# Kernel tuning notes

Hardware: AMD Instinct MI355X
Metric: run time of the kernel (lower is better)

The kernel has to match this reference:

```python
import jax, jax.numpy as jnp
import numpy as np

B, T, D, H = 2, 2048, 1024, 16
DH = D // H


def setup_inputs() -> dict:
    key = jax.random.key(0)
    ks = jax.random.split(key, 5)
    scale = 1.0 / np.sqrt(D)
    return {
        "x": jax.random.normal(ks[0], (B, T, D), dtype=jnp.float32),
        "Wq": jax.random.normal(ks[1], (D, D), dtype=jnp.float32) * scale,
        "Wk": jax.random.normal(ks[2], (D, D), dtype=jnp.float32) * scale,
        "Wv": jax.random.normal(ks[3], (D, D), dtype=jnp.float32) * scale,
        "Wo": jax.random.normal(ks[4], (D, D), dtype=jnp.float32) * scale,
    }


def _split(y):
    # (B,T,D) -> (B,H,T,DH)
    b, t, _ = y.shape
    return y.reshape(b, t, H, DH).transpose(0, 2, 1, 3)


def reference(x, Wq, Wk, Wv, Wo):
    q = _split(x @ Wq)
    k = _split(x @ Wk)
    v = _split(x @ Wv)
    scores = jnp.einsum("bhqd,bhkd->bhqk", q, k) / jnp.sqrt(jnp.float32(DH))
    t = x.shape[1]
    # additive causal mask: -1e9 above the diagonal (matches band_part logic)
    causal = jnp.tril(jnp.ones((t, t), dtype=jnp.float32))
    scores = scores + (1.0 - causal) * -1e9
    attn = jax.nn.softmax(scores, axis=-1)
    out = jnp.einsum("bhqk,bhkd->bhqd", attn, v)  # (B,H,T,DH)
    out = out.transpose(0, 2, 1, 3).reshape(x.shape[0], t, D)
    return out @ Wo
```

## Files before the change

kernel.cpp:

```cpp
#include <hip/hip_runtime.h>

#define BB 2
#define TT 2048
#define DD 1024
#define HH 16
#define DHD 64
#define MM (BB*TT)

typedef __attribute__((ext_vector_type(8))) short short8;
typedef __attribute__((ext_vector_type(4))) float float4v;
typedef unsigned short u16;

__device__ inline float bf2f(u16 u) {
    union { unsigned int i; float f; } v;
    v.i = ((unsigned int)u) << 16;
    return v.f;
}
__device__ inline u16 f2bf(float f) {
    union { float f; unsigned int i; } v;
    v.f = f;
    unsigned int x = v.i;
    unsigned int r = (x + 0x7fffu + ((x >> 16) & 1u)) >> 16;
    return (u16)r;
}

__device__ inline void gl_lds16(const u16* g, u16* l) {
    __builtin_amdgcn_global_load_lds(
        (const __attribute__((address_space(1))) unsigned int*)g,
        (__attribute__((address_space(3))) unsigned int*)l, 16, 0, 0);
}

__global__ __launch_bounds__(256) void prep_k(const float* __restrict__ x,
                                              const float* __restrict__ Wq,
                                              const float* __restrict__ Wk,
                                              const float* __restrict__ Wv,
                                              const float* __restrict__ Wo,
                                              u16* __restrict__ xb,
                                              u16* __restrict__ WT) {
    int tid = threadIdx.x;
    if (blockIdx.z == 4) {
        int bid = blockIdx.y * 32 + blockIdx.x;
#pragma unroll
        for (int k = 0; k < 4; k++) {
            int i = bid * 1024 + k * 256 + tid;
            float4v v = ((const float4v*)x)[i];
            ushort4 o;
            o.x = f2bf(v[0]); o.y = f2bf(v[1]); o.z = f2bf(v[2]); o.w = f2bf(v[3]);
            ((ushort4*)xb)[i] = o;
        }
        return;
    }
    __shared__ u16 t[32][33];
    int wsel = blockIdx.z;
    const float* W = (wsel == 0) ? Wq : (wsel == 1) ? Wk : (wsel == 2) ? Wv : Wo;
    u16* o = WT + (size_t)wsel * DD * DD;
    int k0 = blockIdx.y * 32, n0 = blockIdx.x * 32;
    int tx = tid & 31, ty = tid >> 5;
#pragma unroll
    for (int i = 0; i < 4; i++) {
        int k = ty + i * 8;
        t[k][tx] = f2bf(W[(size_t)(k0 + k) * DD + n0 + tx]);
    }
    __syncthreads();
#pragma unroll
    for (int i = 0; i < 4; i++) {
        int n = ty + i * 8;
        o[(size_t)(n0 + n) * DD + k0 + tx] = t[tx][n];
    }
}

template <int MODE, int TM, int TN, int BK>
__global__ __launch_bounds__(256) void gemm_k(const u16* __restrict__ A,
                                              const u16* __restrict__ WT0,
                                              void* __restrict__ outp) {
    const int K = DD;
    const int MT = TM / 32, NT = TN / 32;
    const int NS = (TM + TN) * (BK / 8) / 256;
    const int CPR = BK / 8;

    int z = blockIdx.z;
    const u16* WT = WT0 + (size_t)z * DD * DD;
    int n0 = blockIdx.x * TN, m0 = blockIdx.y * TM;

    __shared__ u16 S[(TM + TN) * BK];

    int tid = threadIdx.x;
    int lane = tid & 63, w = tid >> 6;
    int wm = (w >> 1) * (TM / 2), wn = (w & 1) * (TN / 2);
    int quad = lane >> 4, l16 = lane & 15;

    const u16* gp[NS];
    u16* lp[NS];
#pragma unroll
    for (int j = 0; j < NS; j++) {
        int cid = tid + j * 256;
        int r = cid / CPR, c = cid % CPR;
        lp[j] = S + (size_t)cid * 8;
        gp[j] = (r < TM ? A + (size_t)(m0 + r) * K
                        : WT + (size_t)(n0 + r - TM) * K) + ((c ^ (r & 7)) * 8);
    }
    int swz = l16 & 7;

    float4v acc[MT][NT];
#pragma unroll
    for (int i = 0; i < MT; i++)
#pragma unroll
        for (int j = 0; j < NT; j++) acc[i][j] = (float4v)(0.0f);

    const int NK = K / BK;
#pragma unroll 1
    for (int ki = 0; ki < NK; ki++) {
        __syncthreads();
#pragma unroll
        for (int j = 0; j < NS; j++)
            gl_lds16(gp[j] + ki * BK, lp[j]);
        __syncthreads();

#pragma unroll
        for (int ks = 0; ks < BK / 32; ks++) {
            int cq = ((ks * 4 + quad) ^ swz) * 8;
            short8 a[MT], b[NT];
#pragma unroll
            for (int mt = 0; mt < MT; mt++)
                a[mt] = *(const short8*)&S[(wm + mt * 16 + l16) * BK + cq];
#pragma unroll
            for (int nt = 0; nt < NT; nt++)
                b[nt] = *(const short8*)&S[(TM + wn + nt * 16 + l16) * BK + cq];
#pragma unroll
            for (int mt = 0; mt < MT; mt++)
#pragma unroll
                for (int nt = 0; nt < NT; nt++)
                    acc[mt][nt] = __builtin_amdgcn_mfma_f32_16x16x32_bf16(
                        a[mt], b[nt], acc[mt][nt], 0, 0, 0);
        }
    }

#pragma unroll
    for (int mt = 0; mt < MT; mt++) {
#pragma unroll
        for (int nt = 0; nt < NT; nt++) {
#pragma unroll
            for (int r = 0; r < 4; r++) {
                int m = m0 + wm + mt * 16 + quad * 4 + r;
                int n = n0 + wn + nt * 16 + l16;
                float v = acc[mt][nt][r];
                if constexpr (MODE == 0) {
                    int bb = m >> 11, t = m & 2047;
                    int h = n >> 6, dh = n & 63;
                    size_t idx;
                    if (z == 2)
                        idx = (((size_t)2 * BB * HH + bb * HH + h) * DHD + dh) * TT + t;
                    else
                        idx = (((size_t)z * BB * HH + bb * HH + h) * TT + t) * DHD + dh;
                    ((u16*)outp)[idx] = f2bf(v);
                } else {
                    ((float*)outp)[(size_t)m * DD + n] = v;
                }
            }
        }
    }
}

__global__ __launch_bounds__(512, 4) void attn_k(const u16* __restrict__ QKV,
                                                 u16* __restrict__ AO) {
    const u16* Q  = QKV;
    const u16* Kp = QKV + (size_t)MM * DD;
    const u16* Vp = QKV + (size_t)2 * MM * DD;
    int bh = blockIdx.x;
    int by = blockIdx.y;
    int qt = (by < 8) ? (15 - by) : (by - 8);
    size_t hoff = (size_t)bh * TT * DHD;

    __shared__ u16 Ks[2][2][64 * 64];
    __shared__ u16 VTs[2][2][64 * 64];
    __shared__ u16 Ps[8][16 * 64];

    int tid = threadIdx.x;
    int lane = tid & 63, wv = tid >> 6;
    int quad = lane >> 4, l16 = lane & 15;
    int cxs = l16 & 7;

    int sr = tid >> 3, sc = tid & 7;
    int sl = sr * 64 + ((sc ^ (sr & 7)) * 8);
    const u16* gK = Kp + hoff + (size_t)sr * DHD + sc * 8;
    const u16* gV = Vp + hoff + (size_t)sr * TT + sc * 8;

    const float qscale = 0.125f * 1.4426950408889634f;
    int q0 = qt * 128;
    int ql = wv * 16 + l16;
    short8 aq0, aq1;
    {
        const u16* gq = Q + hoff + (size_t)(q0 + ql) * DHD;
        short8 v0 = *(const short8*)(gq + quad * 8);
        short8 v1 = *(const short8*)(gq + 32 + quad * 8);
#pragma unroll
        for (int e = 0; e < 8; e++) {
            aq0[e] = (short)f2bf(bf2f((u16)v0[e]) * qscale);
            aq1[e] = (short)f2bf(bf2f((u16)v1[e]) * qscale);
        }
    }

    short8 prK[2], prV[2];
    prK[0] = *(const short8*)gK;
    prK[1] = *(const short8*)(gK + (size_t)64 * DHD);
    prV[0] = *(const short8*)gV;
    prV[1] = *(const short8*)(gV + 64);

    const int NR = qt + 1;

    float4v o[4];
#pragma unroll
    for (int i = 0; i < 4; i++) o[i] = (float4v)(0.0f);
    float lr = 0.0f;

#pragma unroll 1
    for (int jt = 0; jt < NR; jt++) {
        int db = jt & 1;
#pragma unroll
        for (int tt = 0; tt < 2; tt++) {
            *(short8*)&Ks[db][tt][sl]  = prK[tt];
            *(short8*)&VTs[db][tt][sl] = prV[tt];
        }
        __syncthreads();

        if (jt + 1 < NR) {
            size_t nj = (size_t)(jt + 1) * 128;
            prK[0] = *(const short8*)(gK + nj * DHD);
            prK[1] = *(const short8*)(gK + (nj + 64) * DHD);
            prV[0] = *(const short8*)(gV + nj);
            prV[1] = *(const short8*)(gV + nj + 64);
        }

#pragma unroll
        for (int tt = 0; tt < 2; tt++) {
            int lim = ql - tt * 64;
            if (jt == qt && lim < 0) continue;

            float4v s[4];
#pragma unroll
            for (int ct = 0; ct < 4; ct++) {
                int kr = (ct * 16 + l16) * 64;
                short8 ak0 = *(const short8*)&Ks[db][tt][kr + ((quad ^ cxs) * 8)];
                short8 ak1 = *(const short8*)&Ks[db][tt][kr + (((4 + quad) ^ cxs) * 8)];
                float4v sv = (float4v)(0.0f);
                sv = __builtin_amdgcn_mfma_f32_16x16x32_bf16(ak0, aq0, sv, 0, 0, 0);
                sv = __builtin_amdgcn_mfma_f32_16x16x32_bf16(ak1, aq1, sv, 0, 0, 0);
                s[ct] = sv;
            }

            if (jt == qt) {
#pragma unroll
                for (int ct = 0; ct < 4; ct++)
#pragma unroll
                    for (int r = 0; r < 4; r++) {
                        int kvl = ct * 16 + quad * 4 + r;
                        if (kvl > lim) s[ct][r] = -30000.0f;
                    }
            }

#pragma unroll
            for (int ct = 0; ct < 4; ct++) {
                float p0 = __builtin_amdgcn_exp2f(s[ct][0]);
                float p1 = __builtin_amdgcn_exp2f(s[ct][1]);
                float p2 = __builtin_amdgcn_exp2f(s[ct][2]);
                float p3 = __builtin_amdgcn_exp2f(s[ct][3]);
                lr += (p0 + p1) + (p2 + p3);
                union { float f; unsigned u; } c0, c1, c2, c3;
                c0.f = p0; c1.f = p1; c2.f = p2; c3.f = p3;
                ushort4 pw;
                pw.x = (u16)(c0.u >> 16);
                pw.y = (u16)(c1.u >> 16);
                pw.z = (u16)(c2.u >> 16);
                pw.w = (u16)(c3.u >> 16);
                int chnk = (ct * 2 + (quad >> 1)) ^ cxs;
                *(ushort4*)&Ps[wv][l16 * 64 + chnk * 8 + (quad & 1) * 4] = pw;
            }

            short8 ap0 = *(const short8*)&Ps[wv][l16 * 64 + ((quad ^ cxs) * 8)];
            short8 ap1 = *(const short8*)&Ps[wv][l16 * 64 + (((4 + quad) ^ cxs) * 8)];
#pragma unroll
            for (int ct = 0; ct < 4; ct++) {
                int vr = (ct * 16 + l16) * 64;
                short8 bv0 = *(const short8*)&VTs[db][tt][vr + ((quad ^ cxs) * 8)];
                short8 bv1 = *(const short8*)&VTs[db][tt][vr + (((4 + quad) ^ cxs) * 8)];
                o[ct] = __builtin_amdgcn_mfma_f32_16x16x32_bf16(ap0, bv0, o[ct], 0, 0, 0);
                o[ct] = __builtin_amdgcn_mfma_f32_16x16x32_bf16(ap1, bv1, o[ct], 0, 0, 0);
            }
        }
    }

    float rs = lr;
    rs += __shfl_xor(rs, 16);
    rs += __shfl_xor(rs, 32);
    int gbase = lane & 48;
    float rinv[4];
#pragma unroll
    for (int r = 0; r < 4; r++)
        rinv[r] = 1.0f / __shfl(rs, gbase + quad * 4 + r);

    int b = bh >> 4, h = bh & 15;
#pragma unroll
    for (int ct = 0; ct < 4; ct++) {
#pragma unroll
        for (int r = 0; r < 4; r++) {
            int q = q0 + wv * 16 + quad * 4 + r;
            int d = h * 64 + ct * 16 + l16;
            AO[(size_t)(b * TT + q) * DD + d] = f2bf(o[ct][r] * rinv[r]);
        }
    }
}

extern "C" void kernel_launch(void* const* d_in, const int* in_sizes, int n_in,
                              void* d_out, int out_size, void* d_ws, size_t ws_size,
                              hipStream_t stream) {
    const float* x  = (const float*)d_in[0];
    const float* Wq = (const float*)d_in[1];
    const float* Wk = (const float*)d_in[2];
    const float* Wv = (const float*)d_in[3];
    const float* Wo = (const float*)d_in[4];

    u16* xb  = (u16*)d_ws;
    u16* WT  = xb + (size_t)MM * DD;
    u16* QKV = WT + (size_t)4 * DD * DD;
    u16* AO  = QKV + (size_t)3 * MM * DD;
    float* out = (float*)d_out;

    prep_k<<<dim3(32, 32, 5), 256, 0, stream>>>(x, Wq, Wk, Wv, Wo, xb, WT);
    gemm_k<0, 128, 128, 64><<<dim3(DD / 128, MM / 128, 3), 256, 0, stream>>>(xb, WT, QKV);
    attn_k<<<dim3(32, 16), 512, 0, stream>>>(QKV, AO);
    gemm_k<1, 64, 128, 64><<<dim3(DD / 128, MM / 64, 1), 256, 0, stream>>>(AO, WT + (size_t)3 * DD * DD, out);
}
```

Before: 168.8 us.

## Switch attention to 32x32x16 MFMA with register-resident P and KV-split waves

Rewrites the attention inner loop to use 32x32x16 bf16 MFMAs. Each group of four waves handles one 64-key half of the KV tile, and the two groups' partial outputs and row sums are combined through LDS at the end. The probability tile is now rearranged into the A-operand layout with cross-half lane shuffles instead of a round trip through shared memory. This removes the Ps LDS buffer and its writes and reads, and halves the MFMA instruction count. The cost is more accumulator registers, a lower occupancy hint (512,2), and an extra reduction step through LDS.

```diff
diff --git a/kernel.cpp b/kernel.cpp
--- a/kernel.cpp
+++ b/kernel.cpp
@@ -9,6 +9,7 @@
 
 typedef __attribute__((ext_vector_type(8))) short short8;
 typedef __attribute__((ext_vector_type(4))) float float4v;
+typedef __attribute__((ext_vector_type(16))) float f32x16;
 typedef unsigned short u16;
 
 __device__ inline float bf2f(u16 u) {
@@ -22,6 +23,11 @@
     unsigned int x = v.i;
     unsigned int r = (x + 0x7fffu + ((x >> 16) & 1u)) >> 16;
     return (u16)r;
+}
+__device__ inline unsigned packtr(float x, float y) {
+    union { float f; unsigned u; } a, b;
+    a.f = x; b.f = y;
+    return (a.u >> 16) | (b.u & 0xffff0000u);
 }
 
 __device__ inline void gl_lds16(const u16* g, u16* l) {
@@ -161,7 +167,7 @@
     }
 }
 
-__global__ __launch_bounds__(512, 4) void attn_k(const u16* __restrict__ QKV,
+__global__ __launch_bounds__(512, 2) void attn_k(const u16* __restrict__ QKV,
                                                  u16* __restrict__ AO) {
     const u16* Q  = QKV;
     const u16* Kp = QKV + (size_t)MM * DD;
@@ -173,12 +179,12 @@
 
     __shared__ u16 Ks[2][2][64 * 64];
     __shared__ u16 VTs[2][2][64 * 64];
-    __shared__ u16 Ps[8][16 * 64];
 
     int tid = threadIdx.x;
     int lane = tid & 63, wv = tid >> 6;
-    int quad = lane >> 4, l16 = lane & 15;
-    int cxs = l16 & 7;
+    int g = wv >> 2, w4 = wv & 3;
+    int l31 = lane & 31, hi = lane >> 5;
+    int swz = l31 & 7;
 
     int sr = tid >> 3, sc = tid & 7;
     int sl = sr * 64 + ((sc ^ (sr & 7)) * 8);
@@ -187,16 +193,16 @@
 
     const float qscale = 0.125f * 1.4426950408889634f;
     int q0 = qt * 128;
-    int ql = wv * 16 + l16;
-    short8 aq0, aq1;
+    short8 qB[4];
     {
-        const u16* gq = Q + hoff + (size_t)(q0 + ql) * DHD;
-        short8 v0 = *(const short8*)(gq + quad * 8);
-        short8 v1 = *(const short8*)(gq + 32 + quad * 8);
-#pragma unroll
-        for (int e = 0; e < 8; e++) {
-            aq0[e] = (short)f2bf(bf2f((u16)v0[e]) * qscale);
-            aq1[e] = (short)f2bf(bf2f((u16)v1[e]) * qscale);
+        const u16* gq = Q + hoff + (size_t)(q0 + w4 * 32 + l31) * DHD + hi * 8;
+#pragma unroll
+        for (int kt = 0; kt < 4; kt++) {
+            short8 v = *(const short8*)(gq + 16 * kt);
+            short8 sv;
+#pragma unroll
+            for (int e = 0; e < 8; e++) sv[e] = (short)f2bf(bf2f((u16)v[e]) * qscale);
+            qB[kt] = sv;
         }
     }
 
@@ -208,9 +214,7 @@
 
     const int NR = qt + 1;
 
-    float4v o[4];
-#pragma unroll
-    for (int i = 0; i < 4; i++) o[i] = (float4v)(0.0f);
+    f32x16 o0 = (f32x16)(0.0f), o1 = (f32x16)(0.0f);
     float lr = 0.0f;
 
 #pragma unroll 1
@@ -231,81 +235,95 @@
             prV[1] = *(const short8*)(gV + nj + 64);
         }
 
-#pragma unroll
-        for (int tt = 0; tt < 2; tt++) {
-            int lim = ql - tt * 64;
-            if (jt == qt && lim < 0) continue;
-
-            float4v s[4];
-#pragma unroll
-            for (int ct = 0; ct < 4; ct++) {
-                int kr = (ct * 16 + l16) * 64;
-                short8 ak0 = *(const short8*)&Ks[db][tt][kr + ((quad ^ cxs) * 8)];
-                short8 ak1 = *(const short8*)&Ks[db][tt][kr + (((4 + quad) ^ cxs) * 8)];
-                float4v sv = (float4v)(0.0f);
-                sv = __builtin_amdgcn_mfma_f32_16x16x32_bf16(ak0, aq0, sv, 0, 0, 0);
-                sv = __builtin_amdgcn_mfma_f32_16x16x32_bf16(ak1, aq1, sv, 0, 0, 0);
-                s[ct] = sv;
+        f32x16 s0 = (f32x16)(0.0f), s1 = (f32x16)(0.0f);
+#pragma unroll
+        for (int kt = 0; kt < 4; kt++) {
+            int ch = ((hi + 2 * kt) ^ swz) * 8;
+            short8 ak0 = *(const short8*)&Ks[db][g][l31 * 64 + ch];
+            short8 ak1 = *(const short8*)&Ks[db][g][(32 + l31) * 64 + ch];
+            s0 = __builtin_amdgcn_mfma_f32_32x32x16_bf16(ak0, qB[kt], s0, 0, 0, 0);
+            s1 = __builtin_amdgcn_mfma_f32_32x32x16_bf16(ak1, qB[kt], s1, 0, 0, 0);
+        }
+
+        if (jt == qt) {
+            int lim = w4 * 32 + l31 - g * 64;
+#pragma unroll
+            for (int r = 0; r < 16; r++) {
+                int kvl = (r & 3) + 8 * (r >> 2) + 4 * hi;
+                if (kvl > lim) s0[r] = -30000.0f;
+                if (32 + kvl > lim) s1[r] = -30000.0f;
             }
-
-            if (jt == qt) {
-#pragma unroll
-                for (int ct = 0; ct < 4; ct++)
-#pragma unroll
-                    for (int r = 0; r < 4; r++) {
-                        int kvl = ct * 16 + quad * 4 + r;
-                        if (kvl > lim) s[ct][r] = -30000.0f;
-                    }
-            }
-
-#pragma unroll
-            for (int ct = 0; ct < 4; ct++) {
-                float p0 = __builtin_amdgcn_exp2f(s[ct][0]);
-                float p1 = __builtin_amdgcn_exp2f(s[ct][1]);
-                float p2 = __builtin_amdgcn_exp2f(s[ct][2]);
-                float p3 = __builtin_amdgcn_exp2f(s[ct][3]);
-                lr += (p0 + p1) + (p2 + p3);
-                union { float f; unsigned u; } c0, c1, c2, c3;
-                c0.f = p0; c1.f = p1; c2.f = p2; c3.f = p3;
-                ushort4 pw;
-                pw.x = (u16)(c0.u >> 16);
-                pw.y = (u16)(c1.u >> 16);
-                pw.z = (u16)(c2.u >> 16);
-                pw.w = (u16)(c3.u >> 16);
-                int chnk = (ct * 2 + (quad >> 1)) ^ cxs;
-                *(ushort4*)&Ps[wv][l16 * 64 + chnk * 8 + (quad & 1) * 4] = pw;
-            }
-
-            short8 ap0 = *(const short8*)&Ps[wv][l16 * 64 + ((quad ^ cxs) * 8)];
-            short8 ap1 = *(const short8*)&Ps[wv][l16 * 64 + (((4 + quad) ^ cxs) * 8)];
-#pragma unroll
-            for (int ct = 0; ct < 4; ct++) {
-                int vr = (ct * 16 + l16) * 64;
-                short8 bv0 = *(const short8*)&VTs[db][tt][vr + ((quad ^ cxs) * 8)];
-                short8 bv1 = *(const short8*)&VTs[db][tt][vr + (((4 + quad) ^ cxs) * 8)];
-                o[ct] = __builtin_amdgcn_mfma_f32_16x16x32_bf16(ap0, bv0, o[ct], 0, 0, 0);
-                o[ct] = __builtin_amdgcn_mfma_f32_16x16x32_bf16(ap1, bv1, o[ct], 0, 0, 0);
-            }
-        }
-    }
-
-    float rs = lr;
-    rs += __shfl_xor(rs, 16);
-    rs += __shfl_xor(rs, 32);
-    int gbase = lane & 48;
-    float rinv[4];
-#pragma unroll
-    for (int r = 0; r < 4; r++)
-        rinv[r] = 1.0f / __shfl(rs, gbase + quad * 4 + r);
-
-    int b = bh >> 4, h = bh & 15;
-#pragma unroll
-    for (int ct = 0; ct < 4; ct++) {
-#pragma unroll
-        for (int r = 0; r < 4; r++) {
-            int q = q0 + wv * 16 + quad * 4 + r;
-            int d = h * 64 + ct * 16 + l16;
-            AO[(size_t)(b * TT + q) * DD + d] = f2bf(o[ct][r] * rinv[r]);
+        }
+
+#pragma unroll
+        for (int r = 0; r < 16; r++) {
+            s0[r] = __builtin_amdgcn_exp2f(s0[r]);
+            s1[r] = __builtin_amdgcn_exp2f(s1[r]);
+            lr += s0[r] + s1[r];
+        }
+
+        short8 pa[4];
+#pragma unroll
+        for (int kt2 = 0; kt2 < 4; kt2++) {
+            f32x16 ps = (kt2 < 2) ? s0 : s1;
+            const int base = 8 * (kt2 & 1);
+            float e0 = ps[base + 0], e1 = ps[base + 1];
+            float e2 = ps[base + 2], e3 = ps[base + 3];
+            float e4 = ps[base + 4], e5 = ps[base + 5];
+            float e6 = ps[base + 6], e7 = ps[base + 7];
+            unsigned lA = packtr(e0, e1), lB = packtr(e2, e3);
+            unsigned hA = packtr(e4, e5), hB = packtr(e6, e7);
+            unsigned wA = hi ? hA : lA, wB = hi ? hB : lB;
+            unsigned sA = hi ? lA : hA, sB = hi ? lB : hB;
+            unsigned rA = (unsigned)__shfl_xor((int)sA, 32);
+            unsigned rB = (unsigned)__shfl_xor((int)sB, 32);
+            union { unsigned w[4]; short8 v; } u;
+            u.w[0] = hi ? rA : wA; u.w[1] = hi ? rB : wB;
+            u.w[2] = hi ? wA : rA; u.w[3] = hi ? wB : rB;
+            pa[kt2] = u.v;
+        }
+
+#pragma unroll
+        for (int kt2 = 0; kt2 < 4; kt2++) {
+            int ch = ((hi + 2 * kt2) ^ swz) * 8;
+            short8 bv0 = *(const short8*)&VTs[db][g][l31 * 64 + ch];
+            short8 bv1 = *(const short8*)&VTs[db][g][(32 + l31) * 64 + ch];
+            o0 = __builtin_amdgcn_mfma_f32_32x32x16_bf16(pa[kt2], bv0, o0, 0, 0, 0);
+            o1 = __builtin_amdgcn_mfma_f32_32x32x16_bf16(pa[kt2], bv1, o1, 0, 0, 0);
+        }
+    }
+
+    __syncthreads();
+    float* Of = (float*)&Ks[0][0][0];
+    float* Lf = (float*)&VTs[0][0][0];
+    if (g == 1) {
+#pragma unroll
+        for (int r = 0; r < 16; r++) {
+            Of[((w4 * 2 + 0) * 16 + r) * 64 + lane] = o0[r];
+            Of[((w4 * 2 + 1) * 16 + r) * 64 + lane] = o1[r];
+        }
+        Lf[w4 * 64 + lane] = lr;
+    }
+    __syncthreads();
+    if (g == 0) {
+#pragma unroll
+        for (int r = 0; r < 16; r++) {
+            o0[r] += Of[((w4 * 2 + 0) * 16 + r) * 64 + lane];
+            o1[r] += Of[((w4 * 2 + 1) * 16 + r) * 64 + lane];
+        }
+        lr += Lf[w4 * 64 + lane];
+
+        float rs = lr + __shfl_xor(lr, 32);
+
+        int b = bh >> 4, h = bh & 15;
+#pragma unroll
+        for (int r = 0; r < 16; r++) {
+            int qlc = (r & 3) + 8 * (r >> 2) + 4 * hi;
+            float ri = 1.0f / __shfl(rs, qlc);
+            int q = q0 + w4 * 32 + qlc;
+            size_t rb = (size_t)(b * TT + q) * DD + h * 64 + l31;
+            AO[rb]      = f2bf(o0[r] * ri);
+            AO[rb + 32] = f2bf(o1[r] * ri);
         }
     }
 }
```

Result: slower. 175.5 us (+4.0%).
